# Performance work log

Hardware: AMD Instinct MI355X
Metric: run time of the kernel (lower is better)

Reference implementation:

```python
import jax, jax.numpy as jnp
import numpy as np

B, S, DIN, DOUT, E, K = 4, 2048, 1024, 1024, 16, 2


def setup_inputs() -> dict:
    key = jax.random.key(0)
    ks = jax.random.split(key, 6)
    sc = 1.0 / np.sqrt(DIN)
    return {
        "x": jax.random.normal(ks[0], (B, S, DIN), jnp.float32),
        "gate_w": jax.random.uniform(ks[1], (DIN, E), jnp.float32, -sc, sc),
        "gate_b": jax.random.uniform(ks[2], (E,), jnp.float32, -sc, sc),
        "expert_w": jax.random.uniform(ks[3], (E, DIN, DOUT), jnp.float32, -sc, sc),
        "expert_b": jax.random.uniform(ks[4], (E, DOUT), jnp.float32, -sc, sc),
        "expert_biases": jnp.zeros((E,), jnp.float32),
    }


def reference(x, gate_w, gate_b, expert_w, expert_b, expert_biases):
    # gating
    gate_output = x @ gate_w + gate_b                 # [B,S,E]
    gate_probs = jax.nn.sigmoid(gate_output)          # [B,S,E]
    gate_logits = gate_output + expert_biases         # bias-corrected routing logits
    _, top_k_idx = jax.lax.top_k(gate_logits, K)      # [B,S,K] int32
    top_k_probs = jnp.take_along_axis(gate_probs, top_k_idx, axis=-1)  # [B,S,K]
    top_k_probs = top_k_probs / top_k_probs.sum(-1, keepdims=True)

    # dense all-expert compute, as in the original torch.stack
    expert_outputs = jnp.einsum('bsd,edf->ebsf', x, expert_w) + expert_b[:, None, None, :]  # [E,B,S,DOUT]

    # Faithful replication of the torch gather (which, due to the permute,
    # reads channel j (0..K-1) of the selected expert and broadcasts it over DOUT):
    # out[d,b,s,j] = expert_outputs[topk[b,s,j], b, s, j]
    b_ix = jnp.arange(B)[:, None, None]
    s_ix = jnp.arange(S)[None, :, None]
    j_ix = jnp.arange(K)[None, None, :]
    gathered = expert_outputs[top_k_idx, b_ix, s_ix, j_ix]  # [B,S,K]

    final_scalar = (gathered * top_k_probs).sum(-1)          # [B,S]
    final_output = jnp.broadcast_to(final_scalar[..., None], (B, S, DOUT))
    return final_output, gate_probs, top_k_idx
```

## Files before the change

### kernel.cpp

```cpp
#include <hip/hip_runtime.h>
#include <math.h>

#define DIN_  1024
#define DOUT_ 1024
#define NE    16
#define KK    2
#define NTOK  8192


__global__ __launch_bounds__(256) void compact_w_kernel(
    const float* __restrict__ ew,
    float* __restrict__ wc)
{
    int i = blockIdx.x * 256 + threadIdx.x;
    if (i >= NE * KK * DIN_) return;
    int d = i & (DIN_ - 1);
    int j = (i >> 10) & 1;
    int e = i >> 11;
    wc[i] = ew[(size_t)e * DIN_ * DOUT_ + (size_t)d * DOUT_ + j];
}

__global__ __launch_bounds__(256) void gate_kernel(
    const float* __restrict__ x,
    const float* __restrict__ gate_w,
    const float* __restrict__ gate_b,
    const float* __restrict__ ebias,
    float* __restrict__ out_probs,
    float* __restrict__ out_idx,
    float4* __restrict__ ws_rec,
    int write_aux)
{
    __shared__ float red[NE][16][17];
    __shared__ float lgt[16 * NE];

    const int tid = threadIdx.x;
    const int seg = tid >> 4;
    const int tok = tid & 15;
    const int token = blockIdx.x * 16 + tok;

    const float4* x4  = (const float4*)(x + (size_t)token * DIN_) + seg * 16;
    const float4* gw4 = (const float4*)gate_w;

    float acc[NE];
#pragma unroll
    for (int e = 0; e < NE; e++) acc[e] = 0.f;

    for (int i = 0; i < 16; i++) {
        float4 xv = x4[i];
        int d0 = seg * 64 + i * 4;
#pragma unroll
        for (int j = 0; j < 4; j++) {
            int d = d0 + j;
            float xs = (j == 0) ? xv.x : (j == 1) ? xv.y : (j == 2) ? xv.z : xv.w;
            float4 g0 = gw4[d * 4 + 0];
            float4 g1 = gw4[d * 4 + 1];
            float4 g2 = gw4[d * 4 + 2];
            float4 g3 = gw4[d * 4 + 3];
            acc[0]  += xs * g0.x; acc[1]  += xs * g0.y; acc[2]  += xs * g0.z; acc[3]  += xs * g0.w;
            acc[4]  += xs * g1.x; acc[5]  += xs * g1.y; acc[6]  += xs * g1.z; acc[7]  += xs * g1.w;
            acc[8]  += xs * g2.x; acc[9]  += xs * g2.y; acc[10] += xs * g2.z; acc[11] += xs * g2.w;
            acc[12] += xs * g3.x; acc[13] += xs * g3.y; acc[14] += xs * g3.z; acc[15] += xs * g3.w;
        }
    }

#pragma unroll
    for (int e = 0; e < NE; e++) red[e][seg][tok] = acc[e];
    __syncthreads();

    {
        const int rtok = tid >> 4;
        const int e    = tid & 15;
        float s = 0.f;
#pragma unroll
        for (int sg = 0; sg < 16; sg++) s += red[e][sg][rtok];
        s += gate_b[e];
        float prob = 1.f / (1.f + expf(-s));
        int gtoken = blockIdx.x * 16 + rtok;
        if (write_aux) out_probs[(size_t)gtoken * NE + e] = prob;
        lgt[rtok * NE + e] = s;
    }
    __syncthreads();

    if (tid < 16) {
        const int ftok = tid;
        const int gtoken = blockIdx.x * 16 + ftok;
        float go[NE], logit[NE];
#pragma unroll
        for (int e = 0; e < NE; e++) {
            go[e] = lgt[ftok * NE + e];
            logit[e] = go[e] + ebias[e];
        }
        int i0 = 0;
        for (int e = 1; e < NE; e++) if (logit[e] > logit[i0]) i0 = e;
        int i1 = -1;
        for (int e = 0; e < NE; e++) {
            if (e == i0) continue;
            if (i1 < 0 || logit[e] > logit[i1]) i1 = e;
        }
        float p0 = 1.f / (1.f + expf(-go[i0]));
        float p1 = 1.f / (1.f + expf(-go[i1]));
        float inv = 1.f / (p0 + p1);
        if (write_aux) {
            out_idx[(size_t)gtoken * KK + 0] = (float)i0;
            out_idx[(size_t)gtoken * KK + 1] = (float)i1;
        }
        ws_rec[gtoken] = make_float4((float)i0, (float)i1, p0 * inv, p1 * inv);
    }
}

__global__ __launch_bounds__(256) void expert_kernel(
    const float* __restrict__ x,
    const float* __restrict__ wc,
    const float* __restrict__ expert_b,
    const float4* __restrict__ ws_rec,
    float* __restrict__ out_final)
{
    const int wave = threadIdx.x >> 6;
    const int lane = threadIdx.x & 63;
    const int token = blockIdx.x * 4 + wave;

    float4 rec = ws_rec[token];
    int e0 = (int)rec.x;
    int e1 = (int)rec.y;

    const float4* xr = (const float4*)(x + (size_t)token * DIN_);
    const float4* w0 = (const float4*)(wc + ((size_t)e0 * KK + 0) * DIN_);
    const float4* w1 = (const float4*)(wc + ((size_t)e1 * KK + 1) * DIN_);

    float g0 = 0.f, g1 = 0.f;
#pragma unroll
    for (int i = 0; i < 4; i++) {
        float4 xv = xr[i * 64 + lane];
        float4 a  = w0[i * 64 + lane];
        float4 b  = w1[i * 64 + lane];
        g0 += xv.x * a.x + xv.y * a.y + xv.z * a.z + xv.w * a.w;
        g1 += xv.x * b.x + xv.y * b.y + xv.z * b.z + xv.w * b.w;
    }
#pragma unroll
    for (int m = 32; m >= 1; m >>= 1) {
        g0 += __shfl_xor(g0, m, 64);
        g1 += __shfl_xor(g1, m, 64);
    }
    float f = rec.z * (g0 + expert_b[(size_t)e0 * DOUT_ + 0])
            + rec.w * (g1 + expert_b[(size_t)e1 * DOUT_ + 1]);
    float4 fv = make_float4(f, f, f, f);
    float4* o4 = (float4*)(out_final + (size_t)token * DOUT_);
#pragma unroll
    for (int i = 0; i < 4; i++) o4[i * 64 + lane] = fv;
}

extern "C" void kernel_launch(void* const* d_in, const int* in_sizes, int n_in,
                              void* d_out, int out_size, void* d_ws, size_t ws_size,
                              hipStream_t stream) {
    const float* x        = (const float*)d_in[0];
    const float* gate_w   = (const float*)d_in[1];
    const float* gate_b   = (const float*)d_in[2];
    const float* expert_w = (const float*)d_in[3];
    const float* expert_b = (const float*)d_in[4];
    const float* ebias    = (const float*)d_in[5];
    float* out = (float*)d_out;

    float4* ws_rec = (float4*)d_ws;
    float*  wc     = (float*)d_ws + (size_t)NTOK * 4;

    float* out_final = out;
    float* out_probs = out + (size_t)NTOK * DOUT_;
    float* out_idx   = out_probs + (size_t)NTOK * NE;
    int write_aux = (out_size >= NTOK * DOUT_ + NTOK * NE + NTOK * KK) ? 1 : 0;

    compact_w_kernel<<<(NE * KK * DIN_ + 255) / 256, 256, 0, stream>>>(expert_w, wc);
    gate_kernel<<<NTOK / 16, 256, 0, stream>>>(
        x, gate_w, gate_b, ebias, out_probs, out_idx, ws_rec, write_aux);
    expert_kernel<<<NTOK / 4, 256, 0, stream>>>(
        x, wc, expert_b, ws_rec, out_final);
}
```

Before: 158.0 us.

## Fuse gating and expert kernels with x staged in shared memory

Merges the gate and expert kernels into one launch. Each block loads its 16 token rows of x into padded LDS once and reuses them for both the gate dot products and the two expert-channel dot products, so x is read from HBM once instead of twice and the routing record round-trip through global memory goes away. The gate reduction now uses cross-lane shuffles before a smaller LDS reduction, and the weight-compaction kernel reads float2 pairs. In exchange, 64KB+ of LDS per block limits occupancy.

```diff
diff --git a/kernel.cpp b/kernel.cpp
--- a/kernel.cpp
+++ b/kernel.cpp
@@ -6,6 +6,7 @@
 #define NE    16
 #define KK    2
 #define NTOK  8192
+#define RS4   257
 
 
 __global__ __launch_bounds__(256) void compact_w_kernel(
@@ -13,81 +14,104 @@
     float* __restrict__ wc)
 {
     int i = blockIdx.x * 256 + threadIdx.x;
-    if (i >= NE * KK * DIN_) return;
+    if (i >= NE * DIN_) return;
     int d = i & (DIN_ - 1);
-    int j = (i >> 10) & 1;
-    int e = i >> 11;
-    wc[i] = ew[(size_t)e * DIN_ * DOUT_ + (size_t)d * DOUT_ + j];
+    int e = i >> 10;
+    const float2 v = *(const float2*)(ew + (size_t)e * DIN_ * DOUT_ + (size_t)d * DOUT_);
+    wc[(size_t)e * KK * DIN_ + d]        = v.x;
+    wc[(size_t)e * KK * DIN_ + DIN_ + d] = v.y;
 }
 
-__global__ __launch_bounds__(256) void gate_kernel(
+__global__ __launch_bounds__(256) void fused_kernel(
     const float* __restrict__ x,
     const float* __restrict__ gate_w,
     const float* __restrict__ gate_b,
     const float* __restrict__ ebias,
+    const float* __restrict__ wc,
+    const float* __restrict__ expert_b,
+    float* __restrict__ out_final,
     float* __restrict__ out_probs,
     float* __restrict__ out_idx,
-    float4* __restrict__ ws_rec,
     int write_aux)
 {
-    __shared__ float red[NE][16][17];
-    __shared__ float lgt[16 * NE];
+    __shared__ float4 xs[16 * RS4];
+    __shared__ float red2[4][16][17];
+    __shared__ float lgt[16][17];
+    __shared__ float4 recs[16];
 
-    const int tid = threadIdx.x;
+    const int tid  = threadIdx.x;
+    const int wave = tid >> 6;
+    const int lane = tid & 63;
+    const int blk  = blockIdx.x;
+
+    const float4* xg = (const float4*)(x + (size_t)blk * 16 * DIN_);
+#pragma unroll
+    for (int k = 0; k < 16; k++) {
+        int g = k * 256 + tid;
+        xs[(g >> 8) * RS4 + (g & 255)] = xg[g];
+    }
+    __syncthreads();
+
     const int seg = tid >> 4;
     const int tok = tid & 15;
-    const int token = blockIdx.x * 16 + tok;
-
-    const float4* x4  = (const float4*)(x + (size_t)token * DIN_) + seg * 16;
-    const float4* gw4 = (const float4*)gate_w;
+    const float4* xrow = xs + tok * RS4 + seg * 16;
+    const float4* gw4  = (const float4*)gate_w;
 
     float acc[NE];
 #pragma unroll
     for (int e = 0; e < NE; e++) acc[e] = 0.f;
 
     for (int i = 0; i < 16; i++) {
-        float4 xv = x4[i];
+        float4 xv = xrow[i];
         int d0 = seg * 64 + i * 4;
 #pragma unroll
         for (int j = 0; j < 4; j++) {
             int d = d0 + j;
-            float xs = (j == 0) ? xv.x : (j == 1) ? xv.y : (j == 2) ? xv.z : xv.w;
+            float xs_ = (j == 0) ? xv.x : (j == 1) ? xv.y : (j == 2) ? xv.z : xv.w;
             float4 g0 = gw4[d * 4 + 0];
             float4 g1 = gw4[d * 4 + 1];
             float4 g2 = gw4[d * 4 + 2];
             float4 g3 = gw4[d * 4 + 3];
-            acc[0]  += xs * g0.x; acc[1]  += xs * g0.y; acc[2]  += xs * g0.z; acc[3]  += xs * g0.w;
-            acc[4]  += xs * g1.x; acc[5]  += xs * g1.y; acc[6]  += xs * g1.z; acc[7]  += xs * g1.w;
-            acc[8]  += xs * g2.x; acc[9]  += xs * g2.y; acc[10] += xs * g2.z; acc[11] += xs * g2.w;
-            acc[12] += xs * g3.x; acc[13] += xs * g3.y; acc[14] += xs * g3.z; acc[15] += xs * g3.w;
+            acc[0]  += xs_ * g0.x; acc[1]  += xs_ * g0.y; acc[2]  += xs_ * g0.z; acc[3]  += xs_ * g0.w;
+            acc[4]  += xs_ * g1.x; acc[5]  += xs_ * g1.y; acc[6]  += xs_ * g1.z; acc[7]  += xs_ * g1.w;
+            acc[8]  += xs_ * g2.x; acc[9]  += xs_ * g2.y; acc[10] += xs_ * g2.z; acc[11] += xs_ * g2.w;
+            acc[12] += xs_ * g3.x; acc[13] += xs_ * g3.y; acc[14] += xs_ * g3.z; acc[15] += xs_ * g3.w;
         }
     }
 
 #pragma unroll
-    for (int e = 0; e < NE; e++) red[e][seg][tok] = acc[e];
+    for (int e = 0; e < NE; e++) {
+        acc[e] += __shfl_xor(acc[e], 16);
+        acc[e] += __shfl_xor(acc[e], 32);
+    }
+    {
+        const int q = seg & 3;
+#pragma unroll
+        for (int j = 0; j < 4; j++) {
+            int e = q * 4 + j;
+            red2[wave][tok][e] = acc[e];
+        }
+    }
     __syncthreads();
 
     {
         const int rtok = tid >> 4;
         const int e    = tid & 15;
-        float s = 0.f;
-#pragma unroll
-        for (int sg = 0; sg < 16; sg++) s += red[e][sg][rtok];
-        s += gate_b[e];
-        float prob = 1.f / (1.f + expf(-s));
-        int gtoken = blockIdx.x * 16 + rtok;
-        if (write_aux) out_probs[(size_t)gtoken * NE + e] = prob;
-        lgt[rtok * NE + e] = s;
+        float s = red2[0][rtok][e] + red2[1][rtok][e]
+                + red2[2][rtok][e] + red2[3][rtok][e] + gate_b[e];
+        if (write_aux)
+            out_probs[(size_t)(blk * 16 + rtok) * NE + e] = 1.f / (1.f + expf(-s));
+        lgt[rtok][e] = s;
     }
     __syncthreads();
 
     if (tid < 16) {
         const int ftok = tid;
-        const int gtoken = blockIdx.x * 16 + ftok;
+        const int gtoken = blk * 16 + ftok;
         float go[NE], logit[NE];
 #pragma unroll
         for (int e = 0; e < NE; e++) {
-            go[e] = lgt[ftok * NE + e];
+            go[e] = lgt[ftok][e];
             logit[e] = go[e] + ebias[e];
         }
         int i0 = 0;
@@ -104,49 +128,40 @@
             out_idx[(size_t)gtoken * KK + 0] = (float)i0;
             out_idx[(size_t)gtoken * KK + 1] = (float)i1;
         }
-        ws_rec[gtoken] = make_float4((float)i0, (float)i1, p0 * inv, p1 * inv);
+        recs[ftok] = make_float4((float)i0, (float)i1, p0 * inv, p1 * inv);
     }
-}
+    __syncthreads();
 
-__global__ __launch_bounds__(256) void expert_kernel(
-    const float* __restrict__ x,
-    const float* __restrict__ wc,
-    const float* __restrict__ expert_b,
-    const float4* __restrict__ ws_rec,
-    float* __restrict__ out_final)
-{
-    const int wave = threadIdx.x >> 6;
-    const int lane = threadIdx.x & 63;
-    const int token = blockIdx.x * 4 + wave;
-
-    float4 rec = ws_rec[token];
-    int e0 = (int)rec.x;
-    int e1 = (int)rec.y;
-
-    const float4* xr = (const float4*)(x + (size_t)token * DIN_);
-    const float4* w0 = (const float4*)(wc + ((size_t)e0 * KK + 0) * DIN_);
-    const float4* w1 = (const float4*)(wc + ((size_t)e1 * KK + 1) * DIN_);
-
-    float g0 = 0.f, g1 = 0.f;
 #pragma unroll
-    for (int i = 0; i < 4; i++) {
-        float4 xv = xr[i * 64 + lane];
-        float4 a  = w0[i * 64 + lane];
-        float4 b  = w1[i * 64 + lane];
-        g0 += xv.x * a.x + xv.y * a.y + xv.z * a.z + xv.w * a.w;
-        g1 += xv.x * b.x + xv.y * b.y + xv.z * b.z + xv.w * b.w;
+    for (int it = 0; it < 4; it++) {
+        const int lt = wave * 4 + it;
+        float4 rec = recs[lt];
+        int e0 = (int)rec.x;
+        int e1 = (int)rec.y;
+        const float4* xr = xs + lt * RS4;
+        const float4* w0 = (const float4*)(wc + ((size_t)e0 * KK + 0) * DIN_);
+        const float4* w1 = (const float4*)(wc + ((size_t)e1 * KK + 1) * DIN_);
+        float g0 = 0.f, g1 = 0.f;
+#pragma unroll
+        for (int i = 0; i < 4; i++) {
+            float4 xv = xr[i * 64 + lane];
+            float4 a  = w0[i * 64 + lane];
+            float4 b  = w1[i * 64 + lane];
+            g0 += xv.x * a.x + xv.y * a.y + xv.z * a.z + xv.w * a.w;
+            g1 += xv.x * b.x + xv.y * b.y + xv.z * b.z + xv.w * b.w;
+        }
+#pragma unroll
+        for (int m = 32; m >= 1; m >>= 1) {
+            g0 += __shfl_xor(g0, m);
+            g1 += __shfl_xor(g1, m);
+        }
+        float f = rec.z * (g0 + expert_b[(size_t)e0 * DOUT_ + 0])
+                + rec.w * (g1 + expert_b[(size_t)e1 * DOUT_ + 1]);
+        float4 fv = make_float4(f, f, f, f);
+        float4* o4 = (float4*)(out_final + (size_t)(blk * 16 + lt) * DOUT_);
+#pragma unroll
+        for (int i = 0; i < 4; i++) o4[i * 64 + lane] = fv;
     }
-#pragma unroll
-    for (int m = 32; m >= 1; m >>= 1) {
-        g0 += __shfl_xor(g0, m, 64);
-        g1 += __shfl_xor(g1, m, 64);
-    }
-    float f = rec.z * (g0 + expert_b[(size_t)e0 * DOUT_ + 0])
-            + rec.w * (g1 + expert_b[(size_t)e1 * DOUT_ + 1]);
-    float4 fv = make_float4(f, f, f, f);
-    float4* o4 = (float4*)(out_final + (size_t)token * DOUT_);
-#pragma unroll
-    for (int i = 0; i < 4; i++) o4[i * 64 + lane] = fv;
 }
 
 extern "C" void kernel_launch(void* const* d_in, const int* in_sizes, int n_in,
@@ -160,17 +175,15 @@
     const float* ebias    = (const float*)d_in[5];
     float* out = (float*)d_out;
 
-    float4* ws_rec = (float4*)d_ws;
-    float*  wc     = (float*)d_ws + (size_t)NTOK * 4;
+    float* wc = (float*)d_ws;
 
     float* out_final = out;
     float* out_probs = out + (size_t)NTOK * DOUT_;
     float* out_idx   = out_probs + (size_t)NTOK * NE;
     int write_aux = (out_size >= NTOK * DOUT_ + NTOK * NE + NTOK * KK) ? 1 : 0;
 
-    compact_w_kernel<<<(NE * KK * DIN_ + 255) / 256, 256, 0, stream>>>(expert_w, wc);
-    gate_kernel<<<NTOK / 16, 256, 0, stream>>>(
-        x, gate_w, gate_b, ebias, out_probs, out_idx, ws_rec, write_aux);
-    expert_kernel<<<NTOK / 4, 256, 0, stream>>>(
-        x, wc, expert_b, ws_rec, out_final);
+    compact_w_kernel<<<(NE * DIN_ + 255) / 256, 256, 0, stream>>>(expert_w, wc);
+    fused_kernel<<<NTOK / 16, 256, 0, stream>>>(
+        x, gate_w, gate_b, ebias, wc, expert_b,
+        out_final, out_probs, out_idx, write_aux);
 }
```

Result: faster. 148.9 us (-5.8%).
